# Kernel optimization log

Hardware: AMD Instinct MI355X
Metric: run time of the kernel (lower is better)

## Reference

```python
import jax, jax.numpy as jnp
import numpy as np

B = 262144          # batch
D = 128             # feature / hidden width (cfg ind/outd)
OUT = 1             # last layer outd
NE = 5              # five treatment-range experts Q1..Q5
PT = np.array([0.0, 0.2, 0.4, 0.6, 0.8, 1.0], dtype=np.float32)


def setup_inputs() -> dict:
    key = jax.random.key(0)
    ks = jax.random.split(key, 10)
    # x[:,0] = treatment in [0,1), x[:,1:] = features (uniform, matching torch.rand init scale)
    x = jax.random.uniform(ks[0], (B, 1 + D), dtype=jnp.float32)
    # expert params, stacked over the 5 experts; torch init is rand(0,1)
    u = lambda k, shp: jax.random.uniform(k, shp, dtype=jnp.float32)
    return {
        "x": x,
        "W1": u(ks[1], (NE, D, D)),   "tw1": u(ks[2], (NE, 1, D)),   "b1": u(ks[3], (NE, D)),
        "W2": u(ks[4], (NE, D, D)),   "tw2": u(ks[5], (NE, 1, D)),   "b2": u(ks[6], (NE, D)),
        "W3": u(ks[7], (NE, D, OUT)), "tw3": u(ks[8], (NE, 1, OUT)), "b3": u(ks[9], (NE, OUT)),
    }


def reference(x, W1, tw1, b1, W2, tw2, b2, W3, tw3, b3):
    t = x[:, :1]          # [B,1] treatment
    f = x[:, 1:]          # [B,D] features
    out = jnp.zeros((x.shape[0], OUT), dtype=x.dtype)
    for e in range(NE):
        # routing mask: pt[e] <= t < pt[e+1]
        mask = (t >= PT[e]) & (t < PT[e + 1])          # [B,1]
        # expert MLP (Treat_Linear stack): out = f@W + t@tw + b, relu except last
        h = jax.nn.relu(f @ W1[e] + t @ tw1[e] + b1[e])
        h = jax.nn.relu(h @ W2[e] + t @ tw2[e] + b2[e])
        o = h @ W3[e] + t @ tw3[e] + b3[e]             # last layer, no act
        out = out + jnp.where(mask, o, jnp.zeros((), x.dtype))
    return out
```

## Files before the change

kernel.cpp:

```cpp
#include <hip/hip_runtime.h>

#define NROWS 262144
#define NE 5
#define CAP 57344
#define NCH 4096
#define BPE 51
#define CHUNK 256
#define CPAD 16

typedef __attribute__((ext_vector_type(8))) short short8;
typedef __attribute__((ext_vector_type(8))) unsigned short ushort8;
typedef __attribute__((ext_vector_type(4))) float f32x4;

__device__ __forceinline__ unsigned short f2bf(float x) {
  unsigned u = __float_as_uint(x);
  u += 0x7FFF + ((u >> 16) & 1);
  return (unsigned short)(u >> 16);
}
__device__ __forceinline__ int eclass(float t) {
  return (t >= 0.2f) + (t >= 0.4f) + (t >= 0.6f) + (t >= 0.8f);
}

__global__ __launch_bounds__(256) void convw(const float* __restrict__ W1,
                                             const float* __restrict__ W2,
                                             unsigned short* __restrict__ Wswz) {
  int idx = blockIdx.x * 256 + threadIdx.x;
  int which = idx / 81920;
  int rem = idx % 81920;
  int e = rem / 16384;
  int jk = rem % 16384;
  int j = jk >> 7;
  int k = jk & 127;
  const float* W = which ? W2 : W1;
  int byteoff = (j * 256 + k * 2) ^ ((j & 7) << 4);
  Wswz[(size_t)e * 32768 + which * 16384 + (byteoff >> 1)] =
      f2bf(W[(size_t)e * 16384 + k * 128 + j]);
}

__global__ __launch_bounds__(256) void thist(const float* __restrict__ x,
                                             float* __restrict__ tcomp,
                                             int* __restrict__ hist) {
  __shared__ int hS[4][NE];
  int tid = threadIdx.x;
  int r = blockIdx.x * 256 + tid;
  if (tid < 20) hS[tid / NE][tid % NE] = 0;
  float t = x[(size_t)r * 129];
  int e = eclass(t);
  tcomp[r] = t;
  __syncthreads();
  atomicAdd(&hS[tid >> 6][e], 1);
  __syncthreads();
  if (tid < 20) {
    int sub = tid / NE, ee = tid % NE;
    hist[ee * NCH + blockIdx.x * 4 + sub] = hS[sub][ee];
  }
}

__global__ __launch_bounds__(256) void scan(const int* __restrict__ hist,
                                            int* __restrict__ boff,
                                            int* __restrict__ cnt) {
  __shared__ int wsum[4];
  int e = blockIdx.x;
  int tid = threadIdx.x;
  int lane = tid & 63, wv = tid >> 6;

  int v[16];
  int s = 0;
  const int* h = hist + e * NCH + tid * 16;
#pragma unroll
  for (int j = 0; j < 16; ++j) { v[j] = h[j]; s += v[j]; }

  int sc = s;
#pragma unroll
  for (int off = 1; off < 64; off <<= 1) {
    int nv = __shfl_up(sc, off);
    if (lane >= off) sc += nv;
  }
  if (lane == 63) wsum[wv] = sc;
  __syncthreads();
  int wexc = 0;
  for (int k = 0; k < wv; ++k) wexc += wsum[k];
  int run = wexc + sc - s;
  int* bo = boff + e * NCH + tid * 16;
#pragma unroll
  for (int j = 0; j < 16; ++j) { bo[j] = run; run += v[j]; }
  if (tid == 255) cnt[e * CPAD] = run;
}

__global__ __launch_bounds__(256) void compact(
    const float* __restrict__ x, const float* __restrict__ tcomp,
    const int* __restrict__ boff,
    unsigned short* __restrict__ xc, float* __restrict__ tcb,
    int* __restrict__ ridb) {
  __shared__ float xf[64 * 129];
  __shared__ int lcS[NE];
  __shared__ int dstS[64];

  int tid = threadIdx.x;
  int blk = blockIdx.x;
  int r0 = blk * 64;

  if (tid < NE) lcS[tid] = 0;

  float t = 0.f;
  if (tid < 64) t = tcomp[r0 + tid];

  const f32x4* xv = (const f32x4*)(x + (size_t)r0 * 129);
  f32x4* xfv = (f32x4*)xf;
#pragma unroll
  for (int q = 0; q < 8; ++q) xfv[q * 256 + tid] = xv[q * 256 + tid];
  if (tid < 16) xfv[2048 + tid] = xv[2048 + tid];

  if (tid < 64) {
    int e = eclass(t);
    int lp = atomicAdd(&lcS[e], 1);
    int d = e * CAP + min(boff[e * NCH + blk] + lp, CAP - 1);
    dstS[tid] = d;
    tcb[d] = t;
    ridb[d] = r0 + tid;
  }
  __syncthreads();

  int row = tid >> 2;
  int sub = tid & 3;
  int d = dstS[row];
  const float* s = xf + row * 129 + 1 + sub * 32;
  ushort8* dp = (ushort8*)(xc + (size_t)d * 128 + sub * 32);
#pragma unroll
  for (int c = 0; c < 4; ++c) {
    ushort8 pk;
#pragma unroll
    for (int j = 0; j < 8; ++j) pk[j] = f2bf(s[c * 8 + j]);
    dp[c] = pk;
  }
}

__global__ __launch_bounds__(512, 2) void mlp(
    const unsigned short* __restrict__ xc, const float* __restrict__ tcb,
    const int* __restrict__ ridb, const int* __restrict__ cnt,
    const unsigned short* __restrict__ Wswz,
    const float* __restrict__ tw1, const float* __restrict__ b1,
    const float* __restrict__ tw2, const float* __restrict__ b2,
    const float* __restrict__ W3, const float* __restrict__ tw3,
    const float* __restrict__ b3, float* __restrict__ out) {
  __shared__ unsigned short wl[32768];
  __shared__ unsigned short h1[8][32 * 128];

  int tid = threadIdx.x;
  int e = blockIdx.x / BPE;
  int bi = blockIdx.x % BPE;
  int n = min(cnt[e * CPAD], CAP);

  {
    const ushort8* wsrc = (const ushort8*)(Wswz + (size_t)e * 32768);
    ushort8* wdst = (ushort8*)wl;
#pragma unroll
    for (int i = 0; i < 8; ++i) wdst[i * 512 + tid] = wsrc[i * 512 + tid];
  }
  __syncthreads();

  int wave = tid >> 6;
  int lane = tid & 63;
  int lr = lane & 15;
  int lq = lane >> 4;

  const char* wp1 = (const char*)wl;
  const char* wp2 = (const char*)wl + 32768;
  char* hp = (char*)h1[wave];
  const unsigned short* xce = xc + (size_t)e * CAP * 128;
  const float* tce = tcb + (size_t)e * CAP;
  const int* ride = ridb + (size_t)e * CAP;

  int nchunk = (n + CHUNK - 1) / CHUNK;

  auto loada = [&](int cc, short8 (&pa0)[4], short8 (&pa1)[4],
                   float& ptv, int& prv) {
    int base = cc * CHUNK + wave * 32;
    int ci = min(base + (lane & 31), n - 1);
    ptv = tce[ci];
    prv = ride[ci];
    int row0 = min(base + lr, n - 1);
    int row1 = min(base + 16 + lr, n - 1);
#pragma unroll
    for (int ks = 0; ks < 4; ++ks) {
      pa0[ks] = *(const short8*)(xce + (size_t)row0 * 128 + ks * 32 + lq * 8);
      pa1[ks] = *(const short8*)(xce + (size_t)row1 * 128 + ks * 32 + lq * 8);
    }
  };

  short8 a0[4], a1[4];
  float tv; int rv;
  int c = bi;
  if (c < nchunk) loada(c, a0, a1, tv, rv);

  for (; c < nchunk; ) {
    int cn = c + BPE;
    bool hn = (cn < nchunk);
    short8 na0[4], na1[4];
    float ntv = 0.f; int nrv = 0;
    if (hn) loada(cn, na0, na1, ntv, nrv);

    int base = c * CHUNK + wave * 32;

    float t0[4], t1[4];
    int ro0[4], ro1[4];
#pragma unroll
    for (int rr = 0; rr < 4; ++rr) {
      t0[rr] = __shfl(tv, lq * 4 + rr);
      t1[rr] = __shfl(tv, 16 + lq * 4 + rr);
      ro0[rr] = __shfl(rv, lq * 4 + rr);
      ro1[rr] = __shfl(rv, 16 + lq * 4 + rr);
    }

#pragma unroll
    for (int ct = 0; ct < 8; ++ct) {
      int col = ct * 16 + lr;
      short8 b[4];
#pragma unroll
      for (int ks = 0; ks < 4; ++ks) {
        int bo = (col * 256 + ks * 64 + lq * 16) ^ ((lr & 7) << 4);
        b[ks] = *(const short8*)(wp1 + bo);
      }
      f32x4 acc0 = {0.f, 0.f, 0.f, 0.f};
      f32x4 acc1 = {0.f, 0.f, 0.f, 0.f};
#pragma unroll
      for (int ks = 0; ks < 4; ++ks) {
        acc0 = __builtin_amdgcn_mfma_f32_16x16x32_bf16(a0[ks], b[ks], acc0, 0, 0, 0);
        acc1 = __builtin_amdgcn_mfma_f32_16x16x32_bf16(a1[ks], b[ks], acc1, 0, 0, 0);
      }
      float twv = tw1[e * 128 + col];
      float bv  = b1[e * 128 + col];
#pragma unroll
      for (int rr = 0; rr < 4; ++rr) {
        int r0_ = lq * 4 + rr;
        int r1_ = r0_ + 16;
        float v0 = fmaxf(acc0[rr] + t0[rr] * twv + bv, 0.f);
        float v1 = fmaxf(acc1[rr] + t1[rr] * twv + bv, 0.f);
        *(unsigned short*)(hp + ((r0_ * 256 + col * 2) ^ ((r0_ & 7) << 4))) = f2bf(v0);
        *(unsigned short*)(hp + ((r1_ * 256 + col * 2) ^ ((r1_ & 7) << 4))) = f2bf(v1);
      }
    }

    asm volatile("s_waitcnt lgkmcnt(0)" ::: "memory");
    __builtin_amdgcn_sched_barrier(0);

#pragma unroll
    for (int ks = 0; ks < 4; ++ks) {
      int off0 = (lr * 256 + ks * 64 + lq * 16) ^ ((lr & 7) << 4);
      int off1 = ((16 + lr) * 256 + ks * 64 + lq * 16) ^ ((lr & 7) << 4);
      a0[ks] = *(const short8*)(hp + off0);
      a1[ks] = *(const short8*)(hp + off1);
    }

    const float* W3e = W3 + e * 128;
    float o0[4] = {0.f, 0.f, 0.f, 0.f};
    float o1[4] = {0.f, 0.f, 0.f, 0.f};
#pragma unroll
    for (int ct = 0; ct < 8; ++ct) {
      int col = ct * 16 + lr;
      short8 b[4];
#pragma unroll
      for (int ks = 0; ks < 4; ++ks) {
        int bo = (col * 256 + ks * 64 + lq * 16) ^ ((lr & 7) << 4);
        b[ks] = *(const short8*)(wp2 + bo);
      }
      f32x4 acc0 = {0.f, 0.f, 0.f, 0.f};
      f32x4 acc1 = {0.f, 0.f, 0.f, 0.f};
#pragma unroll
      for (int ks = 0; ks < 4; ++ks) {
        acc0 = __builtin_amdgcn_mfma_f32_16x16x32_bf16(a0[ks], b[ks], acc0, 0, 0, 0);
        acc1 = __builtin_amdgcn_mfma_f32_16x16x32_bf16(a1[ks], b[ks], acc1, 0, 0, 0);
      }
      float twv = tw2[e * 128 + col];
      float bv  = b2[e * 128 + col];
      float w3v = W3e[col];
#pragma unroll
      for (int rr = 0; rr < 4; ++rr) {
        float v0 = fmaxf(acc0[rr] + t0[rr] * twv + bv, 0.f);
        float v1 = fmaxf(acc1[rr] + t1[rr] * twv + bv, 0.f);
        o0[rr] += v0 * w3v;
        o1[rr] += v1 * w3v;
      }
    }

#pragma unroll
    for (int rr = 0; rr < 4; ++rr) {
      float s0 = o0[rr], s1 = o1[rr];
      s0 += __shfl_xor(s0, 1);  s1 += __shfl_xor(s1, 1);
      s0 += __shfl_xor(s0, 2);  s1 += __shfl_xor(s1, 2);
      s0 += __shfl_xor(s0, 4);  s1 += __shfl_xor(s1, 4);
      s0 += __shfl_xor(s0, 8);  s1 += __shfl_xor(s1, 8);
      o0[rr] = s0;  o1[rr] = s1;
    }

    if (lr == 0) {
      float tw3v = tw3[e];
      float b3v  = b3[e];
#pragma unroll
      for (int rr = 0; rr < 4; ++rr) {
        if (base + lq * 4 + rr < n)
          out[ro0[rr]] = o0[rr] + t0[rr] * tw3v + b3v;
        if (base + 16 + lq * 4 + rr < n)
          out[ro1[rr]] = o1[rr] + t1[rr] * tw3v + b3v;
      }
    }

    if (hn) {
#pragma unroll
      for (int ks = 0; ks < 4; ++ks) { a0[ks] = na0[ks]; a1[ks] = na1[ks]; }
      tv = ntv; rv = nrv;
    }
    c = cn;
  }
}

extern "C" void kernel_launch(void* const* d_in, const int* in_sizes, int n_in,
                              void* d_out, int out_size, void* d_ws, size_t ws_size,
                              hipStream_t stream) {
  const float* x   = (const float*)d_in[0];
  const float* W1  = (const float*)d_in[1];
  const float* tw1 = (const float*)d_in[2];
  const float* b1  = (const float*)d_in[3];
  const float* W2  = (const float*)d_in[4];
  const float* tw2 = (const float*)d_in[5];
  const float* b2  = (const float*)d_in[6];
  const float* W3  = (const float*)d_in[7];
  const float* tw3 = (const float*)d_in[8];
  const float* b3  = (const float*)d_in[9];
  float* out = (float*)d_out;

  char* ws = (char*)d_ws;
  size_t off = 0;
  int*   cnt   = (int*)(ws + off);   off += 1024;
  float* tcomp = (float*)(ws + off); off += (size_t)NROWS * 4;
  int*   hist  = (int*)(ws + off);   off += (size_t)NE * NCH * 4;
  int*   boff  = (int*)(ws + off);   off += (size_t)NE * NCH * 4;
  int*   ridb  = (int*)(ws + off);   off += (size_t)NE * CAP * 4;
  float* tcb   = (float*)(ws + off); off += (size_t)NE * CAP * 4;
  unsigned short* xc = (unsigned short*)(ws + off); off += (size_t)NE * CAP * 256;
  unsigned short* Wswz = (unsigned short*)(ws + off);

  convw<<<640, 256, 0, stream>>>(W1, W2, Wswz);
  thist<<<NROWS / 256, 256, 0, stream>>>(x, tcomp, hist);
  scan<<<NE, 256, 0, stream>>>(hist, boff, cnt);
  compact<<<NCH, 256, 0, stream>>>(x, tcomp, boff, xc, tcb, ridb);
  mlp<<<NE * BPE, 512, 0, stream>>>(xc, tcb, ridb, cnt, Wswz,
                                    tw1, b1, tw2, b2, W3, tw3, b3, out);
}
```

Before: 98.38 us.

## Drop bf16 compaction buffer; gather fp32 rows directly in MLP via row index

The compact kernel, which copied every row into a per-expert bf16 buffer, is replaced by a lightweight perm kernel that writes only the treatment value and row index per slot. The MLP kernel now gathers fp32 feature rows straight from x through the row index, converts them to bf16 in registers, and prefetches metadata two chunks ahead. This removes a full write and re-read of the compacted feature matrix. In exchange the gathers are unaligned 4-byte-aligned loads of 129-float rows, which are less coalesced, and the conversion work moves into the MLP kernel.

```diff
diff --git a/kernel.cpp b/kernel.cpp
--- a/kernel.cpp
+++ b/kernel.cpp
@@ -11,6 +11,7 @@
 typedef __attribute__((ext_vector_type(8))) short short8;
 typedef __attribute__((ext_vector_type(8))) unsigned short ushort8;
 typedef __attribute__((ext_vector_type(4))) float f32x4;
+typedef __attribute__((ext_vector_type(4), aligned(4))) float f32x4u;
 
 __device__ __forceinline__ unsigned short f2bf(float x) {
   unsigned u = __float_as_uint(x);
@@ -87,56 +88,27 @@
   if (tid == 255) cnt[e * CPAD] = run;
 }
 
-__global__ __launch_bounds__(256) void compact(
-    const float* __restrict__ x, const float* __restrict__ tcomp,
-    const int* __restrict__ boff,
-    unsigned short* __restrict__ xc, float* __restrict__ tcb,
-    int* __restrict__ ridb) {
-  __shared__ float xf[64 * 129];
-  __shared__ int lcS[NE];
-  __shared__ int dstS[64];
-
+__global__ __launch_bounds__(256) void perm(const float* __restrict__ tcomp,
+                                            const int* __restrict__ boff,
+                                            float* __restrict__ tcb,
+                                            int* __restrict__ ridb) {
+  __shared__ int lc[4][NE];
   int tid = threadIdx.x;
   int blk = blockIdx.x;
-  int r0 = blk * 64;
-
-  if (tid < NE) lcS[tid] = 0;
-
-  float t = 0.f;
-  if (tid < 64) t = tcomp[r0 + tid];
-
-  const f32x4* xv = (const f32x4*)(x + (size_t)r0 * 129);
-  f32x4* xfv = (f32x4*)xf;
-#pragma unroll
-  for (int q = 0; q < 8; ++q) xfv[q * 256 + tid] = xv[q * 256 + tid];
-  if (tid < 16) xfv[2048 + tid] = xv[2048 + tid];
-
-  if (tid < 64) {
-    int e = eclass(t);
-    int lp = atomicAdd(&lcS[e], 1);
-    int d = e * CAP + min(boff[e * NCH + blk] + lp, CAP - 1);
-    dstS[tid] = d;
-    tcb[d] = t;
-    ridb[d] = r0 + tid;
-  }
-  __syncthreads();
-
-  int row = tid >> 2;
-  int sub = tid & 3;
-  int d = dstS[row];
-  const float* s = xf + row * 129 + 1 + sub * 32;
-  ushort8* dp = (ushort8*)(xc + (size_t)d * 128 + sub * 32);
-#pragma unroll
-  for (int c = 0; c < 4; ++c) {
-    ushort8 pk;
-#pragma unroll
-    for (int j = 0; j < 8; ++j) pk[j] = f2bf(s[c * 8 + j]);
-    dp[c] = pk;
-  }
+  int r = blk * 256 + tid;
+  int sub = tid >> 6;
+  if (tid < 20) lc[tid / NE][tid % NE] = 0;
+  float t = tcomp[r];
+  int e = eclass(t);
+  __syncthreads();
+  int lp = atomicAdd(&lc[sub][e], 1);
+  int d = e * CAP + min(boff[e * NCH + blk * 4 + sub] + lp, CAP - 1);
+  tcb[d] = t;
+  ridb[d] = r;
 }
 
 __global__ __launch_bounds__(512, 2) void mlp(
-    const unsigned short* __restrict__ xc, const float* __restrict__ tcb,
+    const float* __restrict__ x, const float* __restrict__ tcb,
     const int* __restrict__ ridb, const int* __restrict__ cnt,
     const unsigned short* __restrict__ Wswz,
     const float* __restrict__ tw1, const float* __restrict__ b1,
@@ -167,38 +139,55 @@
   const char* wp1 = (const char*)wl;
   const char* wp2 = (const char*)wl + 32768;
   char* hp = (char*)h1[wave];
-  const unsigned short* xce = xc + (size_t)e * CAP * 128;
   const float* tce = tcb + (size_t)e * CAP;
   const int* ride = ridb + (size_t)e * CAP;
 
   int nchunk = (n + CHUNK - 1) / CHUNK;
 
-  auto loada = [&](int cc, short8 (&pa0)[4], short8 (&pa1)[4],
-                   float& ptv, int& prv) {
-    int base = cc * CHUNK + wave * 32;
-    int ci = min(base + (lane & 31), n - 1);
+  f32x4u fv0[8], fv1[8];
+
+  auto load_meta = [&](int cc, float& ptv, int& prv) {
+    int ci = min(cc * CHUNK + wave * 32 + (lane & 31), n - 1);
     ptv = tce[ci];
     prv = ride[ci];
-    int row0 = min(base + lr, n - 1);
-    int row1 = min(base + 16 + lr, n - 1);
+  };
+  auto issue_fv = [&](int rvX) {
+    int rd0 = __shfl(rvX, lr);
+    int rd1 = __shfl(rvX, 16 + lr);
+    const float* p0 = x + (size_t)rd0 * 129 + 1 + lq * 8;
+    const float* p1 = x + (size_t)rd1 * 129 + 1 + lq * 8;
 #pragma unroll
     for (int ks = 0; ks < 4; ++ks) {
-      pa0[ks] = *(const short8*)(xce + (size_t)row0 * 128 + ks * 32 + lq * 8);
-      pa1[ks] = *(const short8*)(xce + (size_t)row1 * 128 + ks * 32 + lq * 8);
+      fv0[2 * ks]     = *(const f32x4u*)(p0 + ks * 32);
+      fv0[2 * ks + 1] = *(const f32x4u*)(p0 + ks * 32 + 4);
+      fv1[2 * ks]     = *(const f32x4u*)(p1 + ks * 32);
+      fv1[2 * ks + 1] = *(const f32x4u*)(p1 + ks * 32 + 4);
     }
   };
 
-  short8 a0[4], a1[4];
-  float tv; int rv;
+  float tvA = 0.f, tvB = 0.f;
+  int rvA = 0, rvB = 0;
   int c = bi;
-  if (c < nchunk) loada(c, a0, a1, tv, rv);
-
-  for (; c < nchunk; ) {
-    int cn = c + BPE;
-    bool hn = (cn < nchunk);
-    short8 na0[4], na1[4];
-    float ntv = 0.f; int nrv = 0;
-    if (hn) loada(cn, na0, na1, ntv, nrv);
+  if (c < nchunk) load_meta(c, tvA, rvA);
+  if (c + BPE < nchunk) load_meta(c + BPE, tvB, rvB);
+  if (c < nchunk) issue_fv(rvA);
+
+  for (; c < nchunk; c += BPE) {
+    short8 a0[4], a1[4];
+#pragma unroll
+    for (int ks = 0; ks < 4; ++ks) {
+#pragma unroll
+      for (int j = 0; j < 4; ++j) {
+        a0[ks][j]     = (short)f2bf(fv0[2 * ks][j]);
+        a0[ks][4 + j] = (short)f2bf(fv0[2 * ks + 1][j]);
+        a1[ks][j]     = (short)f2bf(fv1[2 * ks][j]);
+        a1[ks][4 + j] = (short)f2bf(fv1[2 * ks + 1][j]);
+      }
+    }
+
+    float tvC = 0.f; int rvC = 0;
+    if (c + 2 * BPE < nchunk) load_meta(c + 2 * BPE, tvC, rvC);
+    if (c + BPE < nchunk) issue_fv(rvB);
 
     int base = c * CHUNK + wave * 32;
 
@@ -206,10 +195,10 @@
     int ro0[4], ro1[4];
 #pragma unroll
     for (int rr = 0; rr < 4; ++rr) {
-      t0[rr] = __shfl(tv, lq * 4 + rr);
-      t1[rr] = __shfl(tv, 16 + lq * 4 + rr);
-      ro0[rr] = __shfl(rv, lq * 4 + rr);
-      ro1[rr] = __shfl(rv, 16 + lq * 4 + rr);
+      t0[rr] = __shfl(tvA, lq * 4 + rr);
+      t1[rr] = __shfl(tvA, 16 + lq * 4 + rr);
+      ro0[rr] = __shfl(rvA, lq * 4 + rr);
+      ro1[rr] = __shfl(rvA, 16 + lq * 4 + rr);
     }
 
 #pragma unroll
@@ -305,12 +294,7 @@
       }
     }
 
-    if (hn) {
-#pragma unroll
-      for (int ks = 0; ks < 4; ++ks) { a0[ks] = na0[ks]; a1[ks] = na1[ks]; }
-      tv = ntv; rv = nrv;
-    }
-    c = cn;
+    tvA = tvB; rvA = rvB; tvB = tvC; rvB = rvC;
   }
 }
 
@@ -337,13 +321,12 @@
   int*   boff  = (int*)(ws + off);   off += (size_t)NE * NCH * 4;
   int*   ridb  = (int*)(ws + off);   off += (size_t)NE * CAP * 4;
   float* tcb   = (float*)(ws + off); off += (size_t)NE * CAP * 4;
-  unsigned short* xc = (unsigned short*)(ws + off); off += (size_t)NE * CAP * 256;
   unsigned short* Wswz = (unsigned short*)(ws + off);
 
   convw<<<640, 256, 0, stream>>>(W1, W2, Wswz);
   thist<<<NROWS / 256, 256, 0, stream>>>(x, tcomp, hist);
   scan<<<NE, 256, 0, stream>>>(hist, boff, cnt);
-  compact<<<NCH, 256, 0, stream>>>(x, tcomp, boff, xc, tcb, ridb);
-  mlp<<<NE * BPE, 512, 0, stream>>>(xc, tcb, ridb, cnt, Wswz,
+  perm<<<NROWS / 256, 256, 0, stream>>>(tcomp, boff, tcb, ridb);
+  mlp<<<NE * BPE, 512, 0, stream>>>(x, tcb, ridb, cnt, Wswz,
                                     tw1, b1, tw2, b2, W3, tw3, b3, out);
 }
```

Result: faster. 94.76 us (-3.7%).

## Split compaction into index permutation and per-expert row gather kernels

Applied to the files above, without the earlier changes.

The single compact kernel, which staged 64 rows of x in shared memory and scattered bf16 rows, is replaced by two kernels. A light perm kernel computes each row's destination slot and writes tcb/ridb. A gatherc kernel then has one thread per compacted row read the source row through unaligned float4 loads, convert it to bf16 and write it contiguously. This turns scattered writes into contiguous writes with gathered reads, and drops the shared-memory staging, at the cost of an extra launch and poorly coalesced per-thread row reads.

```diff
diff --git a/kernel.cpp b/kernel.cpp
--- a/kernel.cpp
+++ b/kernel.cpp
@@ -7,10 +7,12 @@
 #define BPE 51
 #define CHUNK 256
 #define CPAD 16
+#define GBPE 224
 
 typedef __attribute__((ext_vector_type(8))) short short8;
 typedef __attribute__((ext_vector_type(8))) unsigned short ushort8;
 typedef __attribute__((ext_vector_type(4))) float f32x4;
+typedef __attribute__((ext_vector_type(4), aligned(4))) float f32x4u;
 
 __device__ __forceinline__ unsigned short f2bf(float x) {
   unsigned u = __float_as_uint(x);
@@ -87,51 +89,53 @@
   if (tid == 255) cnt[e * CPAD] = run;
 }
 
-__global__ __launch_bounds__(256) void compact(
-    const float* __restrict__ x, const float* __restrict__ tcomp,
-    const int* __restrict__ boff,
-    unsigned short* __restrict__ xc, float* __restrict__ tcb,
-    int* __restrict__ ridb) {
-  __shared__ float xf[64 * 129];
-  __shared__ int lcS[NE];
-  __shared__ int dstS[64];
-
+__global__ __launch_bounds__(256) void perm(const float* __restrict__ tcomp,
+                                            const int* __restrict__ boff,
+                                            float* __restrict__ tcb,
+                                            int* __restrict__ ridb) {
+  __shared__ int lc[4][NE];
   int tid = threadIdx.x;
   int blk = blockIdx.x;
-  int r0 = blk * 64;
-
-  if (tid < NE) lcS[tid] = 0;
-
-  float t = 0.f;
-  if (tid < 64) t = tcomp[r0 + tid];
-
-  const f32x4* xv = (const f32x4*)(x + (size_t)r0 * 129);
-  f32x4* xfv = (f32x4*)xf;
-#pragma unroll
-  for (int q = 0; q < 8; ++q) xfv[q * 256 + tid] = xv[q * 256 + tid];
-  if (tid < 16) xfv[2048 + tid] = xv[2048 + tid];
-
-  if (tid < 64) {
-    int e = eclass(t);
-    int lp = atomicAdd(&lcS[e], 1);
-    int d = e * CAP + min(boff[e * NCH + blk] + lp, CAP - 1);
-    dstS[tid] = d;
-    tcb[d] = t;
-    ridb[d] = r0 + tid;
-  }
-  __syncthreads();
-
-  int row = tid >> 2;
-  int sub = tid & 3;
-  int d = dstS[row];
-  const float* s = xf + row * 129 + 1 + sub * 32;
-  ushort8* dp = (ushort8*)(xc + (size_t)d * 128 + sub * 32);
-#pragma unroll
-  for (int c = 0; c < 4; ++c) {
-    ushort8 pk;
-#pragma unroll
-    for (int j = 0; j < 8; ++j) pk[j] = f2bf(s[c * 8 + j]);
-    dp[c] = pk;
+  int r = blk * 256 + tid;
+  int sub = tid >> 6;
+  if (tid < 20) lc[tid / NE][tid % NE] = 0;
+  float t = tcomp[r];
+  int e = eclass(t);
+  __syncthreads();
+  int lp = atomicAdd(&lc[sub][e], 1);
+  int d = e * CAP + min(boff[e * NCH + blk * 4 + sub] + lp, CAP - 1);
+  tcb[d] = t;
+  ridb[d] = r;
+}
+
+__global__ __launch_bounds__(256) void gatherc(
+    const float* __restrict__ x, const int* __restrict__ ridb,
+    const int* __restrict__ cnt, unsigned short* __restrict__ xc) {
+  int e = blockIdx.x / GBPE;
+  int b = blockIdx.x % GBPE;
+  int n = min(cnt[e * CPAD], CAP);
+  if (b * 256 >= n) return;
+  int d = b * 256 + threadIdx.x;
+  int dd = min(d, n - 1);
+  int r = ridb[e * CAP + dd];
+  const float* src = x + (size_t)r * 129 + 1;
+  unsigned short* dst = xc + (size_t)(e * CAP + dd) * 128;
+
+#pragma unroll
+  for (int half = 0; half < 2; ++half) {
+    f32x4u v[16];
+#pragma unroll
+    for (int q = 0; q < 16; ++q) v[q] = *(const f32x4u*)(src + half * 64 + q * 4);
+#pragma unroll
+    for (int c = 0; c < 8; ++c) {
+      ushort8 pk;
+#pragma unroll
+      for (int j = 0; j < 4; ++j) {
+        pk[j]     = f2bf(v[2 * c][j]);
+        pk[4 + j] = f2bf(v[2 * c + 1][j]);
+      }
+      *(ushort8*)(dst + half * 64 + c * 8) = pk;
+    }
   }
 }
 
@@ -343,7 +347,8 @@
   convw<<<640, 256, 0, stream>>>(W1, W2, Wswz);
   thist<<<NROWS / 256, 256, 0, stream>>>(x, tcomp, hist);
   scan<<<NE, 256, 0, stream>>>(hist, boff, cnt);
-  compact<<<NCH, 256, 0, stream>>>(x, tcomp, boff, xc, tcb, ridb);
+  perm<<<NROWS / 256, 256, 0, stream>>>(tcomp, boff, tcb, ridb);
+  gatherc<<<NE * GBPE, 256, 0, stream>>>(x, ridb, cnt, xc);
   mlp<<<NE * BPE, 512, 0, stream>>>(xc, tcb, ridb, cnt, Wswz,
                                     tw1, b1, tw2, b2, W3, tw3, b3, out);
 }
```

Result: slower. 122.0 us (+24.0%).

## Fuse layer-1 GEMM into compaction kernel and split layer 2 into its own kernel

Applied to the files above, without the earlier changes.

The compaction kernel now also computes the first expert layer. It groups each 64-row block by expert in shared memory, runs the MFMA layer-1 GEMM with W1 read straight from global memory, and writes bf16 hidden activations into the compacted per-expert buffer. The second kernel then handles only layer 2 and the output projection, staging only W2 in LDS, which lets it launch twice as many blocks with higher occupancy. This removes a separate pass of bf16 feature writes and reads. The trade-off is small partial 32-row tiles per block, uncached global weight reads for W1, and scattered 2-byte global stores of h1.

```diff
diff --git a/kernel.cpp b/kernel.cpp
--- a/kernel.cpp
+++ b/kernel.cpp
@@ -4,7 +4,7 @@
 #define NE 5
 #define CAP 57344
 #define NCH 4096
-#define BPE 51
+#define BPE2 102
 #define CHUNK 256
 #define CPAD 16
 
@@ -87,87 +87,179 @@
   if (tid == 255) cnt[e * CPAD] = run;
 }
 
-__global__ __launch_bounds__(256) void compact(
+__global__ __launch_bounds__(256, 3) void l1(
     const float* __restrict__ x, const float* __restrict__ tcomp,
-    const int* __restrict__ boff,
-    unsigned short* __restrict__ xc, float* __restrict__ tcb,
-    int* __restrict__ ridb) {
-  __shared__ float xf[64 * 129];
-  __shared__ int lcS[NE];
-  __shared__ int dstS[64];
+    const int* __restrict__ boff, const unsigned short* __restrict__ Wswz,
+    const float* __restrict__ tw1, const float* __restrict__ b1,
+    float* __restrict__ tcb, int* __restrict__ ridb,
+    unsigned short* __restrict__ h1c) {
+  __shared__ float xf[64 * 128];
+  __shared__ float tS[64];
+  __shared__ int permS[64];
+  __shared__ int cntS[NE];
+  __shared__ int offS[NE];
+  __shared__ int tileE[8], tileB[8], tileN[8];
+  __shared__ int ntS;
 
   int tid = threadIdx.x;
   int blk = blockIdx.x;
   int r0 = blk * 64;
 
-  if (tid < NE) lcS[tid] = 0;
+  if (tid < NE) cntS[tid] = 0;
 
   float t = 0.f;
   if (tid < 64) t = tcomp[r0 + tid];
 
   const f32x4* xv = (const f32x4*)(x + (size_t)r0 * 129);
-  f32x4* xfv = (f32x4*)xf;
-#pragma unroll
-  for (int q = 0; q < 8; ++q) xfv[q * 256 + tid] = xv[q * 256 + tid];
-  if (tid < 16) xfv[2048 + tid] = xv[2048 + tid];
-
+#pragma unroll
+  for (int q = 0; q < 9; ++q) {
+    int v = q * 256 + tid;
+    if (q < 8 || tid < 16) {
+      f32x4 val = xv[v];
+#pragma unroll
+      for (int j = 0; j < 4; ++j) {
+        int l = v * 4 + j;
+        int row = (int)(((unsigned)l * 65028u) >> 23);
+        int c = l - row * 129;
+        if (c == 0) tS[row] = val[j];
+        else        xf[row * 128 + ((c - 1) ^ ((row & 7) << 2))] = val[j];
+      }
+    }
+  }
+
+  int myE = 0, myL = 0;
   if (tid < 64) {
-    int e = eclass(t);
-    int lp = atomicAdd(&lcS[e], 1);
-    int d = e * CAP + min(boff[e * NCH + blk] + lp, CAP - 1);
-    dstS[tid] = d;
+    myE = eclass(t);
+    myL = atomicAdd(&cntS[myE], 1);
+  }
+  __syncthreads();
+
+  if (tid == 0) {
+    int off = 0, nt = 0;
+    for (int e = 0; e < NE; ++e) {
+      offS[e] = off;
+      int ne = cntS[e];
+      for (int s = 0; s < ne; s += 32) {
+        tileE[nt] = e; tileB[nt] = off + s; tileN[nt] = min(32, ne - s); ++nt;
+      }
+      off += ne;
+    }
+    ntS = nt;
+  }
+  __syncthreads();
+
+  if (tid < 64) {
+    permS[offS[myE] + myL] = tid;
+    int d = myE * CAP + min(boff[myE * NCH + blk] + myL, CAP - 1);
     tcb[d] = t;
     ridb[d] = r0 + tid;
   }
   __syncthreads();
 
-  int row = tid >> 2;
-  int sub = tid & 3;
-  int d = dstS[row];
-  const float* s = xf + row * 129 + 1 + sub * 32;
-  ushort8* dp = (ushort8*)(xc + (size_t)d * 128 + sub * 32);
-#pragma unroll
-  for (int c = 0; c < 4; ++c) {
-    ushort8 pk;
-#pragma unroll
-    for (int j = 0; j < 8; ++j) pk[j] = f2bf(s[c * 8 + j]);
-    dp[c] = pk;
-  }
-}
-
-__global__ __launch_bounds__(512, 2) void mlp(
-    const unsigned short* __restrict__ xc, const float* __restrict__ tcb,
-    const int* __restrict__ ridb, const int* __restrict__ cnt,
-    const unsigned short* __restrict__ Wswz,
-    const float* __restrict__ tw1, const float* __restrict__ b1,
-    const float* __restrict__ tw2, const float* __restrict__ b2,
-    const float* __restrict__ W3, const float* __restrict__ tw3,
-    const float* __restrict__ b3, float* __restrict__ out) {
-  __shared__ unsigned short wl[32768];
-  __shared__ unsigned short h1[8][32 * 128];
-
-  int tid = threadIdx.x;
-  int e = blockIdx.x / BPE;
-  int bi = blockIdx.x % BPE;
-  int n = min(cnt[e * CPAD], CAP);
-
-  {
-    const ushort8* wsrc = (const ushort8*)(Wswz + (size_t)e * 32768);
-    ushort8* wdst = (ushort8*)wl;
-#pragma unroll
-    for (int i = 0; i < 8; ++i) wdst[i * 512 + tid] = wsrc[i * 512 + tid];
-  }
-  __syncthreads();
-
+  int numTiles = ntS;
   int wave = tid >> 6;
   int lane = tid & 63;
   int lr = lane & 15;
   int lq = lane >> 4;
 
-  const char* wp1 = (const char*)wl;
-  const char* wp2 = (const char*)wl + 32768;
-  char* hp = (char*)h1[wave];
-  const unsigned short* xce = xc + (size_t)e * CAP * 128;
+  for (int ti = wave; ti < numTiles; ti += 4) {
+    int e  = tileE[ti];
+    int tb = tileB[ti];
+    int tn = tileN[ti];
+    int d0 = e * CAP + min(boff[e * NCH + blk] + (tb - offS[e]), CAP - 64);
+
+    int p0 = permS[tb + min(lr, tn - 1)];
+    int p1 = permS[tb + min(16 + lr, tn - 1)];
+
+    short8 a0[4], a1[4];
+#pragma unroll
+    for (int ks = 0; ks < 4; ++ks) {
+      int cbase = ks * 32 + lq * 8;
+      f32x4 u0 = *(const f32x4*)(xf + p0 * 128 + (cbase ^ ((p0 & 7) << 2)));
+      f32x4 u1 = *(const f32x4*)(xf + p0 * 128 + ((cbase + 4) ^ ((p0 & 7) << 2)));
+      f32x4 w0 = *(const f32x4*)(xf + p1 * 128 + (cbase ^ ((p1 & 7) << 2)));
+      f32x4 w1 = *(const f32x4*)(xf + p1 * 128 + ((cbase + 4) ^ ((p1 & 7) << 2)));
+#pragma unroll
+      for (int j = 0; j < 4; ++j) {
+        a0[ks][j]     = (short)f2bf(u0[j]);
+        a0[ks][4 + j] = (short)f2bf(u1[j]);
+        a1[ks][j]     = (short)f2bf(w0[j]);
+        a1[ks][4 + j] = (short)f2bf(w1[j]);
+      }
+    }
+
+    int pd0[4], pd1[4];
+    float t0[4], t1[4];
+#pragma unroll
+    for (int rr = 0; rr < 4; ++rr) {
+      pd0[rr] = permS[tb + min(lq * 4 + rr, tn - 1)];
+      pd1[rr] = permS[tb + min(16 + lq * 4 + rr, tn - 1)];
+      t0[rr] = tS[pd0[rr]];
+      t1[rr] = tS[pd1[rr]];
+    }
+
+    const char* w1p = (const char*)Wswz + (size_t)e * 65536;
+
+#pragma unroll
+    for (int ct = 0; ct < 8; ++ct) {
+      int col = ct * 16 + lr;
+      short8 b[4];
+#pragma unroll
+      for (int ks = 0; ks < 4; ++ks) {
+        int bo = (col * 256 + ks * 64 + lq * 16) ^ ((lr & 7) << 4);
+        b[ks] = *(const short8*)(w1p + bo);
+      }
+      f32x4 acc0 = {0.f, 0.f, 0.f, 0.f};
+      f32x4 acc1 = {0.f, 0.f, 0.f, 0.f};
+#pragma unroll
+      for (int ks = 0; ks < 4; ++ks) {
+        acc0 = __builtin_amdgcn_mfma_f32_16x16x32_bf16(a0[ks], b[ks], acc0, 0, 0, 0);
+        acc1 = __builtin_amdgcn_mfma_f32_16x16x32_bf16(a1[ks], b[ks], acc1, 0, 0, 0);
+      }
+      float twv = tw1[e * 128 + col];
+      float bv  = b1[e * 128 + col];
+#pragma unroll
+      for (int rr = 0; rr < 4; ++rr) {
+        int s0 = lq * 4 + rr;
+        int s1 = s0 + 16;
+        float v0 = fmaxf(acc0[rr] + t0[rr] * twv + bv, 0.f);
+        float v1 = fmaxf(acc1[rr] + t1[rr] * twv + bv, 0.f);
+        if (s0 < tn) h1c[(size_t)(d0 + s0) * 128 + col] = f2bf(v0);
+        if (s1 < tn) h1c[(size_t)(d0 + s1) * 128 + col] = f2bf(v1);
+      }
+    }
+  }
+}
+
+__global__ __launch_bounds__(512, 4) void l2(
+    const unsigned short* __restrict__ h1c, const float* __restrict__ tcb,
+    const int* __restrict__ ridb, const int* __restrict__ cnt,
+    const unsigned short* __restrict__ Wswz,
+    const float* __restrict__ tw2, const float* __restrict__ b2,
+    const float* __restrict__ W3, const float* __restrict__ tw3,
+    const float* __restrict__ b3, float* __restrict__ out) {
+  __shared__ unsigned short wl[16384];
+
+  int tid = threadIdx.x;
+  int e = blockIdx.x / BPE2;
+  int bi = blockIdx.x % BPE2;
+  int n = min(cnt[e * CPAD], CAP);
+
+  {
+    const ushort8* wsrc = (const ushort8*)(Wswz + (size_t)e * 32768 + 16384);
+    ushort8* wdst = (ushort8*)wl;
+#pragma unroll
+    for (int i = 0; i < 4; ++i) wdst[i * 512 + tid] = wsrc[i * 512 + tid];
+  }
+  __syncthreads();
+
+  int wave = tid >> 6;
+  int lane = tid & 63;
+  int lr = lane & 15;
+  int lq = lane >> 4;
+
+  const char* wp2 = (const char*)wl;
+  const unsigned short* hce = h1c + (size_t)e * CAP * 128;
   const float* tce = tcb + (size_t)e * CAP;
   const int* ride = ridb + (size_t)e * CAP;
 
@@ -183,8 +275,8 @@
     int row1 = min(base + 16 + lr, n - 1);
 #pragma unroll
     for (int ks = 0; ks < 4; ++ks) {
-      pa0[ks] = *(const short8*)(xce + (size_t)row0 * 128 + ks * 32 + lq * 8);
-      pa1[ks] = *(const short8*)(xce + (size_t)row1 * 128 + ks * 32 + lq * 8);
+      pa0[ks] = *(const short8*)(hce + (size_t)row0 * 128 + ks * 32 + lq * 8);
+      pa1[ks] = *(const short8*)(hce + (size_t)row1 * 128 + ks * 32 + lq * 8);
     }
   };
 
@@ -194,7 +286,7 @@
   if (c < nchunk) loada(c, a0, a1, tv, rv);
 
   for (; c < nchunk; ) {
-    int cn = c + BPE;
+    int cn = c + BPE2;
     bool hn = (cn < nchunk);
     short8 na0[4], na1[4];
     float ntv = 0.f; int nrv = 0;
@@ -210,46 +302,6 @@
       t1[rr] = __shfl(tv, 16 + lq * 4 + rr);
       ro0[rr] = __shfl(rv, lq * 4 + rr);
       ro1[rr] = __shfl(rv, 16 + lq * 4 + rr);
-    }
-
-#pragma unroll
-    for (int ct = 0; ct < 8; ++ct) {
-      int col = ct * 16 + lr;
-      short8 b[4];
-#pragma unroll
-      for (int ks = 0; ks < 4; ++ks) {
-        int bo = (col * 256 + ks * 64 + lq * 16) ^ ((lr & 7) << 4);
-        b[ks] = *(const short8*)(wp1 + bo);
-      }
-      f32x4 acc0 = {0.f, 0.f, 0.f, 0.f};
-      f32x4 acc1 = {0.f, 0.f, 0.f, 0.f};
-#pragma unroll
-      for (int ks = 0; ks < 4; ++ks) {
-        acc0 = __builtin_amdgcn_mfma_f32_16x16x32_bf16(a0[ks], b[ks], acc0, 0, 0, 0);
-        acc1 = __builtin_amdgcn_mfma_f32_16x16x32_bf16(a1[ks], b[ks], acc1, 0, 0, 0);
-      }
-      float twv = tw1[e * 128 + col];
-      float bv  = b1[e * 128 + col];
-#pragma unroll
-      for (int rr = 0; rr < 4; ++rr) {
-        int r0_ = lq * 4 + rr;
-        int r1_ = r0_ + 16;
-        float v0 = fmaxf(acc0[rr] + t0[rr] * twv + bv, 0.f);
-        float v1 = fmaxf(acc1[rr] + t1[rr] * twv + bv, 0.f);
-        *(unsigned short*)(hp + ((r0_ * 256 + col * 2) ^ ((r0_ & 7) << 4))) = f2bf(v0);
-        *(unsigned short*)(hp + ((r1_ * 256 + col * 2) ^ ((r1_ & 7) << 4))) = f2bf(v1);
-      }
-    }
-
-    asm volatile("s_waitcnt lgkmcnt(0)" ::: "memory");
-    __builtin_amdgcn_sched_barrier(0);
-
-#pragma unroll
-    for (int ks = 0; ks < 4; ++ks) {
-      int off0 = (lr * 256 + ks * 64 + lq * 16) ^ ((lr & 7) << 4);
-      int off1 = ((16 + lr) * 256 + ks * 64 + lq * 16) ^ ((lr & 7) << 4);
-      a0[ks] = *(const short8*)(hp + off0);
-      a1[ks] = *(const short8*)(hp + off1);
     }
 
     const float* W3e = W3 + e * 128;
@@ -337,13 +389,13 @@
   int*   boff  = (int*)(ws + off);   off += (size_t)NE * NCH * 4;
   int*   ridb  = (int*)(ws + off);   off += (size_t)NE * CAP * 4;
   float* tcb   = (float*)(ws + off); off += (size_t)NE * CAP * 4;
-  unsigned short* xc = (unsigned short*)(ws + off); off += (size_t)NE * CAP * 256;
+  unsigned short* h1c = (unsigned short*)(ws + off); off += (size_t)NE * CAP * 256;
   unsigned short* Wswz = (unsigned short*)(ws + off);
 
   convw<<<640, 256, 0, stream>>>(W1, W2, Wswz);
   thist<<<NROWS / 256, 256, 0, stream>>>(x, tcomp, hist);
   scan<<<NE, 256, 0, stream>>>(hist, boff, cnt);
-  compact<<<NCH, 256, 0, stream>>>(x, tcomp, boff, xc, tcb, ridb);
-  mlp<<<NE * BPE, 512, 0, stream>>>(xc, tcb, ridb, cnt, Wswz,
-                                    tw1, b1, tw2, b2, W3, tw3, b3, out);
-}
+  l1<<<NCH, 256, 0, stream>>>(x, tcomp, boff, Wswz, tw1, b1, tcb, ridb, h1c);
+  l2<<<NE * BPE2, 512, 0, stream>>>(h1c, tcb, ridb, cnt, Wswz,
+                                    tw2, b2, W3, tw3, b3, out);
+}
```

After: 284.0 us. 189% more time.
